# Performance work log

Measured on AMD Instinct MI355X. Metric: run time of the kernel, lower is better.

Reference implementation:

```python
import jax, jax.numpy as jnp
import numpy as np

PROJ = 128
H = 128
G = 2
D = 96
T = 33
NEG = -1e9


def _mlp2(x, W1, b1, W2, b2):
    # Linear -> ReLU -> (Dropout=id in eval) -> Linear -> ReLU
    return jax.nn.relu(jax.nn.relu(x @ W1 + b1) @ W2 + b2)


def _mlp3(x, W1, b1, W2, b2, W3, b3):
    # Linear -> ReLU -> Linear -> ReLU -> Linear
    return jax.nn.relu(jax.nn.relu(x @ W1 + b1) @ W2 + b2) @ W3 + b3


def _init_linear(key, fan_in, fan_out):
    kw, kb = jax.random.split(key)
    bound = 1.0 / np.sqrt(fan_in)
    W = jax.random.uniform(kw, (fan_in, fan_out), jnp.float32, -bound, bound)
    b = jax.random.uniform(kb, (fan_out,), jnp.float32, -bound, bound)
    return W, b


def setup_inputs() -> dict:
    key = jax.random.key(0)
    ks = jax.random.split(key, 16)
    total_T, total_D = G * T, G * D
    x = jax.random.normal(ks[0], (total_T, H, total_D), jnp.float32)
    # sparse block-diagonal weighted adjacency; 0 means no edge
    r = jax.random.uniform(ks[1], (total_D, total_D), jnp.float32, 0.1, 1.0)
    keep = jax.random.uniform(ks[2], (total_D, total_D)) < 0.35
    gid = jnp.repeat(jnp.arange(G), D)
    block = gid[:, None] == gid[None, :]
    edge_w = jnp.where(keep & block, r, 0.0)
    batch = gid.astype(jnp.int64)
    time_i = (jnp.arange(G + 1) * T).astype(jnp.int64)
    ne_W1, ne_b1 = _init_linear(ks[3], H, PROJ)
    ne_W2, ne_b2 = _init_linear(ks[4], PROJ, PROJ)
    ee_W1, ee_b1 = _init_linear(ks[5], 1, PROJ // 4)
    ee_W2, ee_b2 = _init_linear(ks[6], PROJ // 4, PROJ // 4)
    ud_W1, ud_b1 = _init_linear(ks[7], 2 * PROJ + PROJ // 4, PROJ)
    ud_W2, ud_b2 = _init_linear(ks[8], PROJ, PROJ // 2)
    ud_W3, ud_b3 = _init_linear(ks[9], PROJ // 2, 1)
    dp_W1, dp_b1 = _init_linear(ks[10], 2 * PROJ, PROJ)
    dp_W2, dp_b2 = _init_linear(ks[11], PROJ, PROJ // 2)
    dp_W3, dp_b3 = _init_linear(ks[12], PROJ // 2, 1)
    return {
        'x': x, 'edge_w': edge_w, 'batch': batch, 'no_graphs': G, 'time_i': time_i,
        'ne_W1': ne_W1, 'ne_b1': ne_b1, 'ne_W2': ne_W2, 'ne_b2': ne_b2,
        'ee_W1': ee_W1, 'ee_b1': ee_b1, 'ee_W2': ee_W2, 'ee_b2': ee_b2,
        'ud_W1': ud_W1, 'ud_b1': ud_b1, 'ud_W2': ud_W2, 'ud_b2': ud_b2,
        'ud_W3': ud_W3, 'ud_b3': ud_b3,
        'dp_W1': dp_W1, 'dp_b1': dp_b1, 'dp_W2': dp_W2, 'dp_b2': dp_b2,
        'dp_W3': dp_W3, 'dp_b3': dp_b3,
    }


def reference(x, edge_w, batch, no_graphs, time_i,
              ne_W1, ne_b1, ne_W2, ne_b2,
              ee_W1, ee_b1, ee_W2, ee_b2,
              ud_W1, ud_b1, ud_W2, ud_b2, ud_W3, ud_b3,
              dp_W1, dp_b1, dp_W2, dp_b2, dp_W3, dp_b3):
    batch_np = np.asarray(batch)
    time_np = np.asarray(time_i)
    class_out, dist_out = [], []
    start = 0
    for g in range(int(no_graphs)):
        t0, t1 = int(time_np[g]), int(time_np[g + 1])
        idx = np.nonzero(batch_np == g)[0]
        Dg = idx.size
        xg = jnp.take(x[t0:t1], idx, axis=2)                # (T, H, Dg)
        ew = edge_w[start:start + Dg, start:start + Dg]      # (Dg, Dg)
        xc = jnp.transpose(xg[:-1], (0, 2, 1))               # (T-1, Dg, H)
        xn = jnp.transpose(xg[1:], (0, 2, 1))
        xce = _mlp2(xc, ne_W1, ne_b1, ne_W2, ne_b2)          # (T-1, Dg, 128)
        xne = _mlp2(xn, ne_W1, ne_b1, ne_W2, ne_b2)
        ee = _mlp2(ew[..., None], ee_W1, ee_b1, ee_W2, ee_b2)  # (Dg, Dg, 32)
        Tm1 = xce.shape[0]
        feat = jnp.concatenate([
            jnp.broadcast_to(xne[:, :, None, :], (Tm1, Dg, Dg, PROJ)),
            jnp.broadcast_to(xce[:, None, :, :], (Tm1, Dg, Dg, PROJ)),
            jnp.broadcast_to(ee[None], (Tm1, Dg, Dg, PROJ // 4)),
        ], axis=-1)                                          # (T-1, Dg, Dg, 288)
        logits = _mlp3(feat, ud_W1, ud_b1, ud_W2, ud_b2, ud_W3, ud_b3)[..., 0]
        mask = (ew == 0.0) & ~jnp.eye(Dg, dtype=bool)        # non-edge, non-diagonal
        logits = jnp.where(mask[None], NEG, logits)
        dist = _mlp3(jnp.concatenate([xce, xne], axis=-1),
                     dp_W1, dp_b1, dp_W2, dp_b2, dp_W3, dp_b3)[..., 0]
        class_out.append(logits)
        dist_out.append(dist)
        start += Dg
    # all graphs are equal-sized here, so stack the per-graph lists
    return (jnp.stack(class_out), jnp.stack(dist_out))
```

## Files before the change

kernel.cpp:

```cpp
#include <hip/hip_runtime.h>


typedef __bf16 bf16_t;
typedef bf16_t bf16x8 __attribute__((ext_vector_type(8)));
typedef float  f32x4  __attribute__((ext_vector_type(4)));

#define XS_LD 136
#define NEGV  -1000000000.0f

__device__ __forceinline__ bf16x8 gfrag(const float* p, int ld) {
  bf16x8 r;
  #pragma unroll
  for (int m = 0; m < 8; ++m) r[m] = (bf16_t)p[m * ld];
  return r;
}

__global__ __launch_bounds__(256) void kEnc(
    const float* __restrict__ x,
    const float* __restrict__ neW1, const float* __restrict__ neb1,
    const float* __restrict__ neW2, const float* __restrict__ neb2,
    const float* __restrict__ udW1,
    bf16_t* __restrict__ encB, bf16_t* __restrict__ P, bf16_t* __restrict__ Q,
    const float* __restrict__ edge_w,
    const float* __restrict__ eeW1, const float* __restrict__ eeb1,
    const float* __restrict__ eeW2, const float* __restrict__ eeb2,
    bf16_t* __restrict__ E2g) {
  __shared__ bf16_t sX[16 * 136];
  __shared__ bf16_t sH[16 * 136];
  __shared__ bf16_t sE[16 * 136];
  int bid = blockIdx.x, tid = threadIdx.x;
  int l = tid & 63, w = tid >> 6, lr = l & 15, lg = l >> 4;

  if (bid < 396) {
    int ub = bid / 6, mt = bid % 6, g = ub / 33;
    const float* xsrc = x + (size_t)ub * 128 * 192 + g * 96 + mt * 16;
    #pragma unroll
    for (int i = 0; i < 2; ++i) {
      int t = tid + i * 256;
      int h = t >> 2, c4 = (t & 3) * 4;
      f32x4 v = *(const f32x4*)(xsrc + h * 192 + c4);
      #pragma unroll
      for (int r = 0; r < 4; ++r) sX[(c4 + r) * 136 + h] = (bf16_t)v[r];
    }
    __syncthreads();

    {
      bf16x8 a[4];
      #pragma unroll
      for (int ks = 0; ks < 4; ++ks)
        a[ks] = *(const bf16x8*)(sX + lr * 136 + ks * 32 + lg * 8);
      #pragma unroll
      for (int nn = 0; nn < 2; ++nn) {
        int nb = w * 2 + nn;
        bf16x8 bw[4];
        #pragma unroll
        for (int ks = 0; ks < 4; ++ks)
          bw[ks] = gfrag(neW1 + (size_t)(ks*32 + lg*8)*128 + nb*16 + lr, 128);
        f32x4 acc = {0.f,0.f,0.f,0.f};
        #pragma unroll
        for (int ks = 0; ks < 4; ++ks)
          acc = __builtin_amdgcn_mfma_f32_16x16x32_bf16(a[ks], bw[ks], acc, 0, 0, 0);
        float bv = neb1[nb*16 + lr];
        #pragma unroll
        for (int r = 0; r < 4; ++r)
          sH[(lg*4 + r)*136 + nb*16 + lr] = (bf16_t)fmaxf(acc[r] + bv, 0.f);
      }
    }
    __syncthreads();

    bf16_t* encOut = encB + ((size_t)ub * 96 + mt * 16) * 128;
    {
      bf16x8 a[4];
      #pragma unroll
      for (int ks = 0; ks < 4; ++ks)
        a[ks] = *(const bf16x8*)(sH + lr * 136 + ks * 32 + lg * 8);
      #pragma unroll
      for (int nn = 0; nn < 2; ++nn) {
        int nb = w * 2 + nn;
        bf16x8 bw[4];
        #pragma unroll
        for (int ks = 0; ks < 4; ++ks)
          bw[ks] = gfrag(neW2 + (size_t)(ks*32 + lg*8)*128 + nb*16 + lr, 128);
        f32x4 acc = {0.f,0.f,0.f,0.f};
        #pragma unroll
        for (int ks = 0; ks < 4; ++ks)
          acc = __builtin_amdgcn_mfma_f32_16x16x32_bf16(a[ks], bw[ks], acc, 0, 0, 0);
        float bv = neb2[nb*16 + lr];
        #pragma unroll
        for (int r = 0; r < 4; ++r) {
          bf16_t v = (bf16_t)fmaxf(acc[r] + bv, 0.f);
          sE[(lg*4 + r)*136 + nb*16 + lr] = v;
          encOut[(lg*4 + r)*128 + nb*16 + lr] = v;
        }
      }
    }
    __syncthreads();

    {
      bf16x8 a[4];
      #pragma unroll
      for (int ks = 0; ks < 4; ++ks)
        a[ks] = *(const bf16x8*)(sE + lr * 136 + ks * 32 + lg * 8);
      int koff = (w < 2) ? 0 : 128;
      bf16_t* outp = (w < 2) ? P : Q;
      int noff = (w & 1) * 64;
      #pragma unroll
      for (int nb = 0; nb < 4; ++nb) {
        bf16x8 bw[4];
        #pragma unroll
        for (int ks = 0; ks < 4; ++ks)
          bw[ks] = gfrag(udW1 + (size_t)(koff + ks*32 + lg*8)*128 + noff + nb*16 + lr, 128);
        f32x4 acc = {0.f,0.f,0.f,0.f};
        #pragma unroll
        for (int ks = 0; ks < 4; ++ks)
          acc = __builtin_amdgcn_mfma_f32_16x16x32_bf16(a[ks], bw[ks], acc, 0, 0, 0);
        #pragma unroll
        for (int r = 0; r < 4; ++r)
          outp[((size_t)ub*96 + mt*16 + lg*4 + r)*128 + noff + nb*16 + lr] = (bf16_t)acc[r];
      }
    }
  } else {
    int u3 = bid - 396;
    int e0 = u3 * 64 + w * 16;
    int e = e0 + lr;
    int g = e / 9216, rem = e - g * 9216, i = rem / 96, j = rem - i * 96;
    float wv = edge_w[(g*96 + i)*192 + g*96 + j];
    bf16x8 ah;
    #pragma unroll
    for (int m = 0; m < 8; ++m) {
      int k = lg * 8 + m;
      ah[m] = (bf16_t)fmaxf(wv * eeW1[k] + eeb1[k], 0.f);
    }
    #pragma unroll
    for (int nb = 0; nb < 2; ++nb) {
      bf16x8 bw = gfrag(eeW2 + (size_t)(lg*8)*32 + nb*16 + lr, 32);
      f32x4 acc = {0.f,0.f,0.f,0.f};
      acc = __builtin_amdgcn_mfma_f32_16x16x32_bf16(ah, bw, acc, 0, 0, 0);
      float b2 = eeb2[nb*16 + lr];
      #pragma unroll
      for (int r = 0; r < 4; ++r)
        E2g[((size_t)e0 + lg*4 + r)*32 + nb*16 + lr] = (bf16_t)fmaxf(acc[r] + b2, 0.f);
    }
  }
}

__global__ __launch_bounds__(256) void kB(
    const bf16_t* __restrict__ P, const bf16_t* __restrict__ Q,
    const bf16_t* __restrict__ E2g,
    const float* __restrict__ udW1, const float* __restrict__ udW2,
    const float* __restrict__ udb1, const float* __restrict__ udb2,
    const float* __restrict__ udW3, const float* __restrict__ udb3,
    const float* __restrict__ edge_w, float* __restrict__ out_logits,
    const bf16_t* __restrict__ encB,
    const float* __restrict__ dpW1, const float* __restrict__ dpb1,
    const float* __restrict__ dpW2, const float* __restrict__ dpb2,
    const float* __restrict__ dpW3, const float* __restrict__ dpb3,
    float* __restrict__ dist_out) {
  __shared__ bf16_t smem[2 * 64 * XS_LD];
  bf16_t* sb0 = smem;
  bf16_t* sb1 = smem + 64 * XS_LD;
  int b = blockIdx.x, tid = threadIdx.x;
  int l = tid & 63, w = tid >> 6, lr = l & 15, lg = l >> 4;

  if (b < 576) {
    int jt = b % 12, it = (b / 12) % 12, zz = b / 144;
    int g = zz >> 1, th = zz & 1;
    int i0 = it * 8, j0 = jt * 8;
    int e_loc = w * 16 + lr, ii = e_loc >> 3, jj = e_loc & 7;

    bf16x8 wb[4][4];
    #pragma unroll
    for (int nb = 0; nb < 4; ++nb)
      #pragma unroll
      for (int ks = 0; ks < 4; ++ks)
        wb[nb][ks] = gfrag(udW2 + (size_t)(ks*32 + lg*8)*64 + nb*16 + lr, 64);
    float b2v[4], w3v[4], b1v[8];
    #pragma unroll
    for (int nb = 0; nb < 4; ++nb) { b2v[nb] = udb2[nb*16 + lr]; w3v[nb] = udW3[nb*16 + lr]; }
    #pragma unroll
    for (int nb = 0; nb < 8; ++nb) b1v[nb] = udb1[nb*16 + lr];
    float b3 = udb3[0];

    int orow = w*16 + lg*4 + (lr & 3);
    int mi = i0 + (orow >> 3), mj = j0 + (orow & 7);
    float ewv = edge_w[(g*96 + mi)*192 + g*96 + mj];
    bool dead = (ewv == 0.0f) && (mi != mj);

    {
      bf16x8 ae = *(const bf16x8*)(E2g + ((size_t)((g*96 + i0 + ii)*96) + j0 + jj)*32 + lg*8);
      #pragma unroll
      for (int nb = 0; nb < 8; ++nb) {
        bf16x8 bw = gfrag(udW1 + (size_t)(256 + lg*8)*128 + nb*16 + lr, 128);
        f32x4 acc = {0.f,0.f,0.f,0.f};
        acc = __builtin_amdgcn_mfma_f32_16x16x32_bf16(ae, bw, acc, 0, 0, 0);
        #pragma unroll
        for (int r = 0; r < 4; ++r)
          sb0[(w*16 + lg*4 + r)*XS_LD + nb*16 + lr] = (bf16_t)(acc[r] + b1v[nb]);
      }
    }
    __syncthreads();
    float csf[32];
    #pragma unroll
    for (int ks = 0; ks < 4; ++ks) {
      bf16x8 cv = *(const bf16x8*)(sb0 + e_loc*XS_LD + ks*32 + lg*8);
      #pragma unroll
      for (int m = 0; m < 8; ++m) csf[ks*8 + m] = (float)cv[m];
    }

    #pragma unroll 1
    for (int ph = 0; ph < 2; ++ph) {
      int tc = th*2 + ph;
      bf16x8 pst[4], qst[4];
      #pragma unroll
      for (int r = 0; r < 4; ++r) {
        int c = tid + r * 256;
        int row = c >> 4, kc = c & 15;
        int tt = row >> 3, rr = row & 7;
        pst[r] = *(const bf16x8*)(P + ((size_t)((g*33 + tc*8 + tt + 1)*96) + i0 + rr)*128 + kc*8);
        qst[r] = *(const bf16x8*)(Q + ((size_t)((g*33 + tc*8 + tt)*96) + j0 + rr)*128 + kc*8);
      }
      __syncthreads();
      #pragma unroll
      for (int r = 0; r < 4; ++r) {
        int c = tid + r * 256;
        int row = c >> 4, kc = c & 15;
        *(bf16x8*)(sb0 + row*XS_LD + kc*8) = pst[r];
        *(bf16x8*)(sb1 + row*XS_LD + kc*8) = qst[r];
      }
      __syncthreads();

      #pragma unroll 2
      for (int tt = 0; tt < 8; ++tt) {
        int prow = tt*8 + ii, qrow = tt*8 + jj;
        bf16x8 a[4];
        #pragma unroll
        for (int ks = 0; ks < 4; ++ks) {
          bf16x8 pv = *(const bf16x8*)(sb0 + prow*XS_LD + ks*32 + lg*8);
          bf16x8 qv = *(const bf16x8*)(sb1 + qrow*XS_LD + ks*32 + lg*8);
          #pragma unroll
          for (int m = 0; m < 8; ++m) {
            float s = (float)pv[m] + (float)qv[m] + csf[ks*8 + m];
            a[ks][m] = (bf16_t)fmaxf(s, 0.f);
          }
        }
        f32x4 acc[4];
        #pragma unroll
        for (int nb = 0; nb < 4; ++nb) {
          f32x4 t4 = {0.f,0.f,0.f,0.f};
          #pragma unroll
          for (int ks = 0; ks < 4; ++ks)
            t4 = __builtin_amdgcn_mfma_f32_16x16x32_bf16(a[ks], wb[nb][ks], t4, 0, 0, 0);
          acc[nb] = t4;
        }
        float partial[4];
        #pragma unroll
        for (int r = 0; r < 4; ++r) {
          float ps = 0.f;
          #pragma unroll
          for (int nb = 0; nb < 4; ++nb)
            ps += fmaxf(acc[nb][r] + b2v[nb], 0.f) * w3v[nb];
          partial[r] = ps;
        }
        #pragma unroll
        for (int r = 0; r < 4; ++r) {
          partial[r] += __shfl_xor(partial[r], 1, 16);
          partial[r] += __shfl_xor(partial[r], 2, 16);
          partial[r] += __shfl_xor(partial[r], 4, 16);
          partial[r] += __shfl_xor(partial[r], 8, 16);
        }
        if (lr < 4) {
          float v = (lr == 0) ? partial[0] : (lr == 1) ? partial[1]
                  : (lr == 2) ? partial[2] : partial[3];
          v = dead ? NEGV : (v + b3);
          out_logits[(size_t)((g*32 + tc*8 + tt)*96 + mi)*96 + mj] = v;
        }
      }
    }
  } else {
    int u = b - 576;
    int g = u >> 6, t = (u >> 1) & 31, half = u & 1;
    int r0 = half * 48;
    if (w < 3) {
      bf16x8 a[8];
      #pragma unroll
      for (int ks = 0; ks < 8; ++ks) {
        int h2 = ks >> 2;
        int kk = (ks & 3)*32 + lg*8;
        a[ks] = *(const bf16x8*)(encB + (size_t)((g*33 + t + h2)*96 + r0 + w*16 + lr)*128 + kk);
      }
      #pragma unroll
      for (int nb = 0; nb < 8; ++nb) {
        f32x4 acc = {0.f,0.f,0.f,0.f};
        #pragma unroll
        for (int ks = 0; ks < 8; ++ks) {
          bf16x8 bfr = gfrag(dpW1 + (size_t)(ks*32 + lg*8)*128 + nb*16 + lr, 128);
          acc = __builtin_amdgcn_mfma_f32_16x16x32_bf16(a[ks], bfr, acc, 0, 0, 0);
        }
        int n = nb*16 + lr; float bv = dpb1[n];
        #pragma unroll
        for (int r = 0; r < 4; ++r)
          sb0[(w*16 + lg*4 + r)*XS_LD + n] = (bf16_t)fmaxf(acc[r] + bv, 0.f);
      }
    }
    __syncthreads();
    if (w < 3) {
      bf16x8 a2[4];
      #pragma unroll
      for (int ks = 0; ks < 4; ++ks)
        a2[ks] = *(const bf16x8*)(sb0 + (w*16 + lr)*XS_LD + ks*32 + lg*8);
      f32x4 acc[4];
      #pragma unroll
      for (int nb = 0; nb < 4; ++nb) {
        f32x4 t4 = {0.f,0.f,0.f,0.f};
        #pragma unroll
        for (int ks = 0; ks < 4; ++ks) {
          bf16x8 bfr = gfrag(dpW2 + (size_t)(ks*32 + lg*8)*64 + nb*16 + lr, 64);
          t4 = __builtin_amdgcn_mfma_f32_16x16x32_bf16(a2[ks], bfr, t4, 0, 0, 0);
        }
        acc[nb] = t4;
      }
      float b2v[4], w3v[4];
      #pragma unroll
      for (int nb = 0; nb < 4; ++nb) { b2v[nb] = dpb2[nb*16 + lr]; w3v[nb] = dpW3[nb*16 + lr]; }
      float partial[4];
      #pragma unroll
      for (int r = 0; r < 4; ++r) {
        float ps = 0.f;
        #pragma unroll
        for (int nb = 0; nb < 4; ++nb)
          ps += fmaxf(acc[nb][r] + b2v[nb], 0.f) * w3v[nb];
        partial[r] = ps;
      }
      #pragma unroll
      for (int r = 0; r < 4; ++r) {
        partial[r] += __shfl_xor(partial[r], 1, 16);
        partial[r] += __shfl_xor(partial[r], 2, 16);
        partial[r] += __shfl_xor(partial[r], 4, 16);
        partial[r] += __shfl_xor(partial[r], 8, 16);
      }
      if (lr < 4) {
        float v = (lr == 0) ? partial[0] : (lr == 1) ? partial[1]
                : (lr == 2) ? partial[2] : partial[3];
        v += dpb3[0];
        int row = r0 + w*16 + lg*4 + lr;
        dist_out[(size_t)(g*32 + t)*96 + row] = v;
      }
    }
  }
}

extern "C" void kernel_launch(void* const* d_in, const int* in_sizes, int n_in,
                              void* d_out, int out_size, void* d_ws, size_t ws_size,
                              hipStream_t stream) {
  (void)in_sizes; (void)n_in; (void)out_size; (void)ws_size;
  const float* x      = (const float*)d_in[0];
  const float* edge_w = (const float*)d_in[1];
  const float* neW1 = (const float*)d_in[5];
  const float* neb1 = (const float*)d_in[6];
  const float* neW2 = (const float*)d_in[7];
  const float* neb2 = (const float*)d_in[8];
  const float* eeW1 = (const float*)d_in[9];
  const float* eeb1 = (const float*)d_in[10];
  const float* eeW2 = (const float*)d_in[11];
  const float* eeb2 = (const float*)d_in[12];
  const float* udW1 = (const float*)d_in[13];
  const float* udb1 = (const float*)d_in[14];
  const float* udW2 = (const float*)d_in[15];
  const float* udb2 = (const float*)d_in[16];
  const float* udW3 = (const float*)d_in[17];
  const float* udb3 = (const float*)d_in[18];
  const float* dpW1 = (const float*)d_in[19];
  const float* dpb1 = (const float*)d_in[20];
  const float* dpW2 = (const float*)d_in[21];
  const float* dpb2 = (const float*)d_in[22];
  const float* dpW3 = (const float*)d_in[23];
  const float* dpb3 = (const float*)d_in[24];

  char* ws = (char*)d_ws;
  size_t off = 0;
  auto alloc = [&](size_t bytes) -> char* {
    off = (off + 255) & ~(size_t)255;
    char* p = ws + off;
    off += bytes;
    return p;
  };
  bf16_t* encB   = (bf16_t*)alloc((size_t)2*33*96*128 * 2);
  bf16_t* Pbuf   = (bf16_t*)alloc((size_t)2*33*96*128 * 2);
  bf16_t* Qbuf   = (bf16_t*)alloc((size_t)2*33*96*128 * 2);
  bf16_t* E2g    = (bf16_t*)alloc((size_t)2*96*96*32  * 2);

  float* out_logits = (float*)d_out;
  float* dist_out   = (float*)d_out + 2*32*96*96;

  kEnc<<<dim3(684), dim3(256), 0, stream>>>(
      x, neW1, neb1, neW2, neb2, udW1, encB, Pbuf, Qbuf,
      edge_w, eeW1, eeb1, eeW2, eeb2, E2g);

  kB<<<dim3(704), dim3(256), 0, stream>>>(
      Pbuf, Qbuf, E2g, udW1, udW2, udb1, udb2, udW3, udb3, edge_w, out_logits,
      encB, dpW1, dpb1, dpW2, dpb2, dpW3, dpb3, dist_out);
}
```

Before: 155.6 us.

## Precompute edge projection and transposed bf16 weights in encoder, split kB per time-chunk

The edge-feature projection through the udW1 edge slice (plus bias) moves from kB into the encoder kernel and is written to a global Csg buffer. New encoder blocks also pre-transpose udW2, dpW1 and dpW2 into bf16 so kB can load weight fragments with single vector loads instead of strided scalar gathers. kB now assigns one time-chunk per block (1152 blocks instead of 576 blocks looping twice), and issues the P/Q global loads before the weight setup to overlap latency. The cost is a larger intermediate buffer (128 channels per edge instead of 32), extra global traffic, and redundant per-block setup across twice as many blocks.

```diff
diff --git a/kernel.cpp b/kernel.cpp
--- a/kernel.cpp
+++ b/kernel.cpp
@@ -19,19 +19,24 @@
     const float* __restrict__ x,
     const float* __restrict__ neW1, const float* __restrict__ neb1,
     const float* __restrict__ neW2, const float* __restrict__ neb2,
-    const float* __restrict__ udW1,
+    const float* __restrict__ udW1, const float* __restrict__ udb1,
     bf16_t* __restrict__ encB, bf16_t* __restrict__ P, bf16_t* __restrict__ Q,
     const float* __restrict__ edge_w,
     const float* __restrict__ eeW1, const float* __restrict__ eeb1,
     const float* __restrict__ eeW2, const float* __restrict__ eeb2,
-    bf16_t* __restrict__ E2g) {
-  __shared__ bf16_t sX[16 * 136];
-  __shared__ bf16_t sH[16 * 136];
-  __shared__ bf16_t sE[16 * 136];
+    bf16_t* __restrict__ Csg,
+    const float* __restrict__ udW2, const float* __restrict__ dpW1,
+    const float* __restrict__ dpW2,
+    bf16_t* __restrict__ udW2T, bf16_t* __restrict__ dpW1T,
+    bf16_t* __restrict__ dpW2T) {
+  __shared__ char smem[16640];
   int bid = blockIdx.x, tid = threadIdx.x;
   int l = tid & 63, w = tid >> 6, lr = l & 15, lg = l >> 4;
 
   if (bid < 396) {
+    bf16_t* sX = (bf16_t*)smem;
+    bf16_t* sH = (bf16_t*)smem + 16 * 136;
+    bf16_t* sE = (bf16_t*)smem + 32 * 136;
     int ub = bid / 6, mt = bid % 6, g = ub / 33;
     const float* xsrc = x + (size_t)ub * 128 * 192 + g * 96 + mt * 16;
     #pragma unroll
@@ -119,10 +124,11 @@
           outp[((size_t)ub*96 + mt*16 + lg*4 + r)*128 + noff + nb*16 + lr] = (bf16_t)acc[r];
       }
     }
-  } else {
+  } else if (bid < 684) {
+    bf16_t* sE2 = (bf16_t*)smem;
     int u3 = bid - 396;
-    int e0 = u3 * 64 + w * 16;
-    int e = e0 + lr;
+    int e0b = u3 * 64;
+    int e = e0b + w * 16 + lr;
     int g = e / 9216, rem = e - g * 9216, i = rem / 96, j = rem - i * 96;
     float wv = edge_w[(g*96 + i)*192 + g*96 + j];
     bf16x8 ah;
@@ -139,21 +145,54 @@
       float b2 = eeb2[nb*16 + lr];
       #pragma unroll
       for (int r = 0; r < 4; ++r)
-        E2g[((size_t)e0 + lg*4 + r)*32 + nb*16 + lr] = (bf16_t)fmaxf(acc[r] + b2, 0.f);
+        sE2[(w*16 + lg*4 + r)*40 + nb*16 + lr] = (bf16_t)fmaxf(acc[r] + b2, 0.f);
+    }
+    __syncthreads();
+    bf16x8 ae = *(const bf16x8*)(sE2 + (w*16 + lr)*40 + lg*8);
+    #pragma unroll
+    for (int nb = 0; nb < 8; ++nb) {
+      bf16x8 bw = gfrag(udW1 + (size_t)(256 + lg*8)*128 + nb*16 + lr, 128);
+      f32x4 acc = {0.f,0.f,0.f,0.f};
+      acc = __builtin_amdgcn_mfma_f32_16x16x32_bf16(ae, bw, acc, 0, 0, 0);
+      float b1 = udb1[nb*16 + lr];
+      #pragma unroll
+      for (int r = 0; r < 4; ++r)
+        Csg[((size_t)e0b + w*16 + lg*4 + r)*128 + nb*16 + lr] = (bf16_t)(acc[r] + b1);
+    }
+  } else {
+    static const unsigned char tS[12]  = {0,0, 1,1,1,1,1,1,1,1, 2,2};
+    static const short tLdS[12] = {64,64, 128,128,128,128,128,128,128,128, 64,64};
+    static const short tLdD[12] = {128,128, 256,256,256,256,256,256,256,256, 128,128};
+    static const short tR0[12]  = {0,64, 0,0,64,64,128,128,192,192, 0,64};
+    static const short tC0[12]  = {0,0, 0,64,0,64,0,64,0,64, 0,0};
+    int u = bid - 684;
+    const float* S = (tS[u] == 0) ? udW2 : (tS[u] == 1) ? dpW1 : dpW2;
+    bf16_t* Dst = (tS[u] == 0) ? udW2T : (tS[u] == 1) ? dpW1T : dpW2T;
+    int ldS = tLdS[u], ldD = tLdD[u], r0 = tR0[u], c0 = tC0[u];
+    float (*tile)[65] = (float(*)[65])smem;
+    #pragma unroll
+    for (int i = 0; i < 16; ++i) {
+      int idx = tid + i * 256, r = idx >> 6, c = idx & 63;
+      tile[r][c] = S[(r0 + r) * ldS + c0 + c];
+    }
+    __syncthreads();
+    #pragma unroll
+    for (int i = 0; i < 16; ++i) {
+      int idx = tid + i * 256, n = idx >> 6, k = idx & 63;
+      Dst[(c0 + n) * ldD + r0 + k] = (bf16_t)tile[k][n];
     }
   }
 }
 
 __global__ __launch_bounds__(256) void kB(
     const bf16_t* __restrict__ P, const bf16_t* __restrict__ Q,
-    const bf16_t* __restrict__ E2g,
-    const float* __restrict__ udW1, const float* __restrict__ udW2,
-    const float* __restrict__ udb1, const float* __restrict__ udb2,
+    const bf16_t* __restrict__ Csg, const bf16_t* __restrict__ udW2T,
+    const float* __restrict__ udb2,
     const float* __restrict__ udW3, const float* __restrict__ udb3,
     const float* __restrict__ edge_w, float* __restrict__ out_logits,
     const bf16_t* __restrict__ encB,
-    const float* __restrict__ dpW1, const float* __restrict__ dpb1,
-    const float* __restrict__ dpW2, const float* __restrict__ dpb2,
+    const bf16_t* __restrict__ dpW1T, const float* __restrict__ dpb1,
+    const bf16_t* __restrict__ dpW2T, const float* __restrict__ dpb2,
     const float* __restrict__ dpW3, const float* __restrict__ dpb3,
     float* __restrict__ dist_out) {
   __shared__ bf16_t smem[2 * 64 * XS_LD];
@@ -162,23 +201,38 @@
   int b = blockIdx.x, tid = threadIdx.x;
   int l = tid & 63, w = tid >> 6, lr = l & 15, lg = l >> 4;
 
-  if (b < 576) {
-    int jt = b % 12, it = (b / 12) % 12, zz = b / 144;
-    int g = zz >> 1, th = zz & 1;
+  if (b < 1152) {
+    int jt = b % 12, it = (b / 12) % 12, z = b / 144;
+    int g = z >> 2, tc = z & 3;
     int i0 = it * 8, j0 = jt * 8;
     int e_loc = w * 16 + lr, ii = e_loc >> 3, jj = e_loc & 7;
 
+    bf16x8 pst[4], qst[4];
+    #pragma unroll
+    for (int r = 0; r < 4; ++r) {
+      int c = tid + r * 256;
+      int row = c >> 4, kc = c & 15;
+      int tt = row >> 3, rr = row & 7;
+      pst[r] = *(const bf16x8*)(P + ((size_t)((g*33 + tc*8 + tt + 1)*96) + i0 + rr)*128 + kc*8);
+      qst[r] = *(const bf16x8*)(Q + ((size_t)((g*33 + tc*8 + tt)*96) + j0 + rr)*128 + kc*8);
+    }
+    int eg = g*9216 + (i0 + ii)*96 + j0 + jj;
+    float csf[32];
+    #pragma unroll
+    for (int ks = 0; ks < 4; ++ks) {
+      bf16x8 cv = *(const bf16x8*)(Csg + (size_t)eg*128 + ks*32 + lg*8);
+      #pragma unroll
+      for (int m = 0; m < 8; ++m) csf[ks*8 + m] = (float)cv[m];
+    }
     bf16x8 wb[4][4];
     #pragma unroll
     for (int nb = 0; nb < 4; ++nb)
       #pragma unroll
       for (int ks = 0; ks < 4; ++ks)
-        wb[nb][ks] = gfrag(udW2 + (size_t)(ks*32 + lg*8)*64 + nb*16 + lr, 64);
-    float b2v[4], w3v[4], b1v[8];
+        wb[nb][ks] = *(const bf16x8*)(udW2T + (nb*16 + lr)*128 + ks*32 + lg*8);
+    float b2v[4], w3v[4];
     #pragma unroll
     for (int nb = 0; nb < 4; ++nb) { b2v[nb] = udb2[nb*16 + lr]; w3v[nb] = udW3[nb*16 + lr]; }
-    #pragma unroll
-    for (int nb = 0; nb < 8; ++nb) b1v[nb] = udb1[nb*16 + lr];
     float b3 = udb3[0];
 
     int orow = w*16 + lg*4 + (lr & 3);
@@ -186,98 +240,63 @@
     float ewv = edge_w[(g*96 + mi)*192 + g*96 + mj];
     bool dead = (ewv == 0.0f) && (mi != mj);
 
-    {
-      bf16x8 ae = *(const bf16x8*)(E2g + ((size_t)((g*96 + i0 + ii)*96) + j0 + jj)*32 + lg*8);
-      #pragma unroll
-      for (int nb = 0; nb < 8; ++nb) {
-        bf16x8 bw = gfrag(udW1 + (size_t)(256 + lg*8)*128 + nb*16 + lr, 128);
-        f32x4 acc = {0.f,0.f,0.f,0.f};
-        acc = __builtin_amdgcn_mfma_f32_16x16x32_bf16(ae, bw, acc, 0, 0, 0);
-        #pragma unroll
-        for (int r = 0; r < 4; ++r)
-          sb0[(w*16 + lg*4 + r)*XS_LD + nb*16 + lr] = (bf16_t)(acc[r] + b1v[nb]);
-      }
-    }
-    __syncthreads();
-    float csf[32];
-    #pragma unroll
-    for (int ks = 0; ks < 4; ++ks) {
-      bf16x8 cv = *(const bf16x8*)(sb0 + e_loc*XS_LD + ks*32 + lg*8);
-      #pragma unroll
-      for (int m = 0; m < 8; ++m) csf[ks*8 + m] = (float)cv[m];
-    }
-
-    #pragma unroll 1
-    for (int ph = 0; ph < 2; ++ph) {
-      int tc = th*2 + ph;
-      bf16x8 pst[4], qst[4];
+    #pragma unroll
+    for (int r = 0; r < 4; ++r) {
+      int c = tid + r * 256;
+      int row = c >> 4, kc = c & 15;
+      *(bf16x8*)(sb0 + row*XS_LD + kc*8) = pst[r];
+      *(bf16x8*)(sb1 + row*XS_LD + kc*8) = qst[r];
+    }
+    __syncthreads();
+
+    #pragma unroll 2
+    for (int tt = 0; tt < 8; ++tt) {
+      int prow = tt*8 + ii, qrow = tt*8 + jj;
+      bf16x8 a[4];
+      #pragma unroll
+      for (int ks = 0; ks < 4; ++ks) {
+        bf16x8 pv = *(const bf16x8*)(sb0 + prow*XS_LD + ks*32 + lg*8);
+        bf16x8 qv = *(const bf16x8*)(sb1 + qrow*XS_LD + ks*32 + lg*8);
+        #pragma unroll
+        for (int m = 0; m < 8; ++m) {
+          float s = (float)pv[m] + (float)qv[m] + csf[ks*8 + m];
+          a[ks][m] = (bf16_t)fmaxf(s, 0.f);
+        }
+      }
+      f32x4 acc[4];
+      #pragma unroll
+      for (int nb = 0; nb < 4; ++nb) {
+        f32x4 t4 = {0.f,0.f,0.f,0.f};
+        #pragma unroll
+        for (int ks = 0; ks < 4; ++ks)
+          t4 = __builtin_amdgcn_mfma_f32_16x16x32_bf16(a[ks], wb[nb][ks], t4, 0, 0, 0);
+        acc[nb] = t4;
+      }
+      float partial[4];
       #pragma unroll
       for (int r = 0; r < 4; ++r) {
-        int c = tid + r * 256;
-        int row = c >> 4, kc = c & 15;
-        int tt = row >> 3, rr = row & 7;
-        pst[r] = *(const bf16x8*)(P + ((size_t)((g*33 + tc*8 + tt + 1)*96) + i0 + rr)*128 + kc*8);
-        qst[r] = *(const bf16x8*)(Q + ((size_t)((g*33 + tc*8 + tt)*96) + j0 + rr)*128 + kc*8);
-      }
-      __syncthreads();
+        float ps = 0.f;
+        #pragma unroll
+        for (int nb = 0; nb < 4; ++nb)
+          ps += fmaxf(acc[nb][r] + b2v[nb], 0.f) * w3v[nb];
+        partial[r] = ps;
+      }
       #pragma unroll
       for (int r = 0; r < 4; ++r) {
-        int c = tid + r * 256;
-        int row = c >> 4, kc = c & 15;
-        *(bf16x8*)(sb0 + row*XS_LD + kc*8) = pst[r];
-        *(bf16x8*)(sb1 + row*XS_LD + kc*8) = qst[r];
-      }
-      __syncthreads();
-
-      #pragma unroll 2
-      for (int tt = 0; tt < 8; ++tt) {
-        int prow = tt*8 + ii, qrow = tt*8 + jj;
-        bf16x8 a[4];
-        #pragma unroll
-        for (int ks = 0; ks < 4; ++ks) {
-          bf16x8 pv = *(const bf16x8*)(sb0 + prow*XS_LD + ks*32 + lg*8);
-          bf16x8 qv = *(const bf16x8*)(sb1 + qrow*XS_LD + ks*32 + lg*8);
-          #pragma unroll
-          for (int m = 0; m < 8; ++m) {
-            float s = (float)pv[m] + (float)qv[m] + csf[ks*8 + m];
-            a[ks][m] = (bf16_t)fmaxf(s, 0.f);
-          }
-        }
-        f32x4 acc[4];
-        #pragma unroll
-        for (int nb = 0; nb < 4; ++nb) {
-          f32x4 t4 = {0.f,0.f,0.f,0.f};
-          #pragma unroll
-          for (int ks = 0; ks < 4; ++ks)
-            t4 = __builtin_amdgcn_mfma_f32_16x16x32_bf16(a[ks], wb[nb][ks], t4, 0, 0, 0);
-          acc[nb] = t4;
-        }
-        float partial[4];
-        #pragma unroll
-        for (int r = 0; r < 4; ++r) {
-          float ps = 0.f;
-          #pragma unroll
-          for (int nb = 0; nb < 4; ++nb)
-            ps += fmaxf(acc[nb][r] + b2v[nb], 0.f) * w3v[nb];
-          partial[r] = ps;
-        }
-        #pragma unroll
-        for (int r = 0; r < 4; ++r) {
-          partial[r] += __shfl_xor(partial[r], 1, 16);
-          partial[r] += __shfl_xor(partial[r], 2, 16);
-          partial[r] += __shfl_xor(partial[r], 4, 16);
-          partial[r] += __shfl_xor(partial[r], 8, 16);
-        }
-        if (lr < 4) {
-          float v = (lr == 0) ? partial[0] : (lr == 1) ? partial[1]
-                  : (lr == 2) ? partial[2] : partial[3];
-          v = dead ? NEGV : (v + b3);
-          out_logits[(size_t)((g*32 + tc*8 + tt)*96 + mi)*96 + mj] = v;
-        }
+        partial[r] += __shfl_xor(partial[r], 1, 16);
+        partial[r] += __shfl_xor(partial[r], 2, 16);
+        partial[r] += __shfl_xor(partial[r], 4, 16);
+        partial[r] += __shfl_xor(partial[r], 8, 16);
+      }
+      if (lr < 4) {
+        float v = (lr == 0) ? partial[0] : (lr == 1) ? partial[1]
+                : (lr == 2) ? partial[2] : partial[3];
+        v = dead ? NEGV : (v + b3);
+        out_logits[(size_t)((g*32 + tc*8 + tt)*96 + mi)*96 + mj] = v;
       }
     }
   } else {
-    int u = b - 576;
+    int u = b - 1152;
     int g = u >> 6, t = (u >> 1) & 31, half = u & 1;
     int r0 = half * 48;
     if (w < 3) {
@@ -293,7 +312,7 @@
         f32x4 acc = {0.f,0.f,0.f,0.f};
         #pragma unroll
         for (int ks = 0; ks < 8; ++ks) {
-          bf16x8 bfr = gfrag(dpW1 + (size_t)(ks*32 + lg*8)*128 + nb*16 + lr, 128);
+          bf16x8 bfr = *(const bf16x8*)(dpW1T + (size_t)(nb*16 + lr)*256 + ks*32 + lg*8);
           acc = __builtin_amdgcn_mfma_f32_16x16x32_bf16(a[ks], bfr, acc, 0, 0, 0);
         }
         int n = nb*16 + lr; float bv = dpb1[n];
@@ -314,7 +333,7 @@
         f32x4 t4 = {0.f,0.f,0.f,0.f};
         #pragma unroll
         for (int ks = 0; ks < 4; ++ks) {
-          bf16x8 bfr = gfrag(dpW2 + (size_t)(ks*32 + lg*8)*64 + nb*16 + lr, 64);
+          bf16x8 bfr = *(const bf16x8*)(dpW2T + (nb*16 + lr)*128 + ks*32 + lg*8);
           t4 = __builtin_amdgcn_mfma_f32_16x16x32_bf16(a2[ks], bfr, t4, 0, 0, 0);
         }
         acc[nb] = t4;
@@ -387,16 +406,20 @@
   bf16_t* encB   = (bf16_t*)alloc((size_t)2*33*96*128 * 2);
   bf16_t* Pbuf   = (bf16_t*)alloc((size_t)2*33*96*128 * 2);
   bf16_t* Qbuf   = (bf16_t*)alloc((size_t)2*33*96*128 * 2);
-  bf16_t* E2g    = (bf16_t*)alloc((size_t)2*96*96*32  * 2);
+  bf16_t* Csg    = (bf16_t*)alloc((size_t)2*96*96*128 * 2);
+  bf16_t* udW2T  = (bf16_t*)alloc(8192  * 2);
+  bf16_t* dpW1T  = (bf16_t*)alloc(32768 * 2);
+  bf16_t* dpW2T  = (bf16_t*)alloc(8192  * 2);
 
   float* out_logits = (float*)d_out;
   float* dist_out   = (float*)d_out + 2*32*96*96;
 
-  kEnc<<<dim3(684), dim3(256), 0, stream>>>(
-      x, neW1, neb1, neW2, neb2, udW1, encB, Pbuf, Qbuf,
-      edge_w, eeW1, eeb1, eeW2, eeb2, E2g);
-
-  kB<<<dim3(704), dim3(256), 0, stream>>>(
-      Pbuf, Qbuf, E2g, udW1, udW2, udb1, udb2, udW3, udb3, edge_w, out_logits,
-      encB, dpW1, dpb1, dpW2, dpb2, dpW3, dpb3, dist_out);
+  kEnc<<<dim3(696), dim3(256), 0, stream>>>(
+      x, neW1, neb1, neW2, neb2, udW1, udb1, encB, Pbuf, Qbuf,
+      edge_w, eeW1, eeb1, eeW2, eeb2, Csg,
+      udW2, dpW1, dpW2, udW2T, dpW1T, dpW2T);
+
+  kB<<<dim3(1280), dim3(256), 0, stream>>>(
+      Pbuf, Qbuf, Csg, udW2T, udb2, udW3, udb3, edge_w, out_logits,
+      encB, dpW1T, dpb1, dpW2T, dpb2, dpW3, dpb3, dist_out);
 }
```

Measured after the change: 149.4 us. 1.04x faster.
